# Kernel optimization log

Hardware: AMD Instinct MI355X
Metric: run time of the kernel (lower is better)

Reference implementation:

```python
import jax, jax.numpy as jnp
import numpy as np

N_NODES = 50000


def setup_inputs() -> dict:
    key = jax.random.key(0)
    k1, k2, k3, k4 = jax.random.split(key, 4)
    in_f, out_f = 128, 128
    n_edges = 625000
    x = jax.random.normal(k1, (N_NODES, in_f), dtype=jnp.float32)
    index = jax.random.randint(k2, (2, n_edges), 0, N_NODES, dtype=jnp.int64)
    # reset_parameters uses uniform(-1/sqrt(in), 1/sqrt(in))
    bound = 1.0 / np.sqrt(in_f)
    weight = jax.random.uniform(k3, (in_f, out_f), minval=-bound, maxval=bound, dtype=jnp.float32)
    bias = jax.random.uniform(k4, (out_f,), minval=-bound, maxval=bound, dtype=jnp.float32)
    return {"x": x, "index": index, "weight": weight, "bias": bias}


def reference(x, index, weight, bias):
    # F_out = D_hat^{-1/2} (A + I) D_hat^{-1/2} X W + b
    n = x.shape[0]
    loops = jnp.arange(n, dtype=index.dtype)
    src = jnp.concatenate([index[0], loops])  # [E + N]
    dst = jnp.concatenate([index[1], loops])
    # degrees of A_hat (counted on destination nodes)
    deg = jax.ops.segment_sum(jnp.ones_like(dst, dtype=x.dtype), dst, num_segments=n)
    dinv = jax.lax.rsqrt(jnp.maximum(deg, 1e-12))
    norm = dinv[src] * dinv[dst]  # [E + N]
    h = x @ weight  # [N, out] dense GEMM first (out <= in)
    msg = h[src] * norm[:, None]  # gather + scale
    out = jax.ops.segment_sum(msg, dst, num_segments=n)  # scatter-add
    return out + bias
```

## Files before the change

### kernel.cpp

```cpp
#include <hip/hip_runtime.h>

#define F    128
#define PAD  64
#define BKB  1024

typedef short short8 __attribute__((ext_vector_type(8)));
typedef float f32x4v __attribute__((ext_vector_type(4)));

__device__ __forceinline__ ushort f2bf(float f) {
    uint b = __float_as_uint(f);
    uint r = (b + 0x7fffu + ((b >> 16) & 1u)) >> 16;
    return (ushort)r;
}
__device__ __forceinline__ float bflo(uint v) { return __uint_as_float(v << 16); }
__device__ __forceinline__ float bfhi(uint v) { return __uint_as_float(v & 0xffff0000u); }


__global__ __launch_bounds__(256) void bucket(
    const int* __restrict__ src, const int* __restrict__ dst, int ne,
    int* __restrict__ cnt, ushort* __restrict__ padded, int n)
{
    const int xcd   = blockIdx.x & 7;
    const int slice = blockIdx.x >> 3;
    const int nsl   = BKB >> 3;
    int chunk = ((ne + nsl - 1) / nsl + 3) & ~3;
    const int sh  = (n + 7) >> 3;
    const int dlo = xcd * sh;
    const int dhi = (dlo + sh) < n ? (dlo + sh) : n;
    const int base = slice * chunk;
    const int lim  = (base + chunk) < ne ? (base + chunk) : ne;

    for (int e0 = base + threadIdx.x * 4; e0 < lim; e0 += 1024) {
        if (e0 + 3 < lim) {
            int4 s4 = *reinterpret_cast<const int4*>(&src[e0]);
            int4 d4 = *reinterpret_cast<const int4*>(&dst[e0]);
            if (d4.x >= dlo && d4.x < dhi) {
                int p = atomicAdd(&cnt[d4.x], 1);
                if (p < PAD) padded[(size_t)d4.x * PAD + p] = (ushort)s4.x;
            }
            if (d4.y >= dlo && d4.y < dhi) {
                int p = atomicAdd(&cnt[d4.y], 1);
                if (p < PAD) padded[(size_t)d4.y * PAD + p] = (ushort)s4.y;
            }
            if (d4.z >= dlo && d4.z < dhi) {
                int p = atomicAdd(&cnt[d4.z], 1);
                if (p < PAD) padded[(size_t)d4.z * PAD + p] = (ushort)s4.z;
            }
            if (d4.w >= dlo && d4.w < dhi) {
                int p = atomicAdd(&cnt[d4.w], 1);
                if (p < PAD) padded[(size_t)d4.w * PAD + p] = (ushort)s4.w;
            }
        } else {
            for (int e = e0; e < lim; ++e) {
                int d = dst[e];
                if (d >= dlo && d < dhi) {
                    int p = atomicAdd(&cnt[d], 1);
                    if (p < PAD) padded[(size_t)d * PAD + p] = (ushort)src[e];
                }
            }
        }
    }
}


__global__ __launch_bounds__(256) void gemm(
    const float* __restrict__ x, const float* __restrict__ w,
    ushort* __restrict__ g, int n)
{
    const int t    = threadIdx.x;
    const int lane = t & 63;
    const int wv   = t >> 6;
    const int wr   = wv >> 1, wc = wv & 1;
    const int l15  = lane & 15, kg = lane >> 4;
    const int row0 = blockIdx.x * 64 + wr * 32;
    const int col0 = wc * 64;

    f32x4v acc[2][4];
    #pragma unroll
    for (int rt = 0; rt < 2; ++rt)
        #pragma unroll
        for (int ct = 0; ct < 4; ++ct)
            acc[rt][ct] = (f32x4v){0.f, 0.f, 0.f, 0.f};

    #pragma unroll
    for (int kt = 0; kt < 4; ++kt) {
        const int k0 = kt * 32 + kg * 8;
        short8 a[2];
        #pragma unroll
        for (int rt = 0; rt < 2; ++rt) {
            int row = row0 + rt * 16 + l15;
            row = row < n ? row : n - 1;
            float4 p0 = *reinterpret_cast<const float4*>(&x[(size_t)row * F + k0]);
            float4 p1 = *reinterpret_cast<const float4*>(&x[(size_t)row * F + k0 + 4]);
            ushort u[8] = {f2bf(p0.x), f2bf(p0.y), f2bf(p0.z), f2bf(p0.w),
                           f2bf(p1.x), f2bf(p1.y), f2bf(p1.z), f2bf(p1.w)};
            a[rt] = *reinterpret_cast<short8*>(u);
        }
        short8 b[4];
        #pragma unroll
        for (int ct = 0; ct < 4; ++ct) {
            int col = col0 + ct * 16 + l15;
            ushort u[8];
            #pragma unroll
            for (int j = 0; j < 8; ++j)
                u[j] = f2bf(w[(size_t)(k0 + j) * F + col]);
            b[ct] = *reinterpret_cast<short8*>(u);
        }
        #pragma unroll
        for (int rt = 0; rt < 2; ++rt)
            #pragma unroll
            for (int ct = 0; ct < 4; ++ct)
                acc[rt][ct] = __builtin_amdgcn_mfma_f32_16x16x32_bf16(
                    a[rt], b[ct], acc[rt][ct], 0, 0, 0);
    }

    #pragma unroll
    for (int rt = 0; rt < 2; ++rt) {
        int rbase = row0 + rt * 16 + kg * 4;
        #pragma unroll
        for (int ct = 0; ct < 4; ++ct) {
            int col = col0 + ct * 16 + l15;
            #pragma unroll
            for (int rr = 0; rr < 4; ++rr) {
                int row = rbase + rr;
                if (row < n)
                    g[(size_t)row * F + col] = f2bf(acc[rt][ct][rr]);
            }
        }
    }
}


__global__ __launch_bounds__(256) void gather_bf16(
    const int* __restrict__ cnt, const ushort* __restrict__ padded,
    const ushort* __restrict__ g, const float* __restrict__ bias,
    float* __restrict__ out, int n)
{
    int wid  = (blockIdx.x * 256 + threadIdx.x) >> 6;
    int lane = threadIdx.x & 63;
    if (wid >= n) return;
    wid = __builtin_amdgcn_readfirstlane(wid);
    const int c = lane * 2;

    int   cv = cnt[wid];
    float dv = rsqrtf((float)cv + 1.0f);
    uint self = *reinterpret_cast<const uint*>(&g[(size_t)wid * F + c]);
    float ax = dv * bflo(self), ay = dv * bfhi(self);

    int m = cv < PAD ? cv : PAD;
    const ushort* pl = padded + (size_t)wid * PAD;

    int j = 0;
    for (; j + 4 <= m; j += 4) {
        int s0 = pl[j + 0], s1 = pl[j + 1], s2 = pl[j + 2], s3 = pl[j + 3];
        float d0 = rsqrtf((float)cnt[s0] + 1.0f);
        float d1 = rsqrtf((float)cnt[s1] + 1.0f);
        float d2 = rsqrtf((float)cnt[s2] + 1.0f);
        float d3 = rsqrtf((float)cnt[s3] + 1.0f);
        uint v0 = *reinterpret_cast<const uint*>(&g[(size_t)s0 * F + c]);
        uint v1 = *reinterpret_cast<const uint*>(&g[(size_t)s1 * F + c]);
        uint v2 = *reinterpret_cast<const uint*>(&g[(size_t)s2 * F + c]);
        uint v3 = *reinterpret_cast<const uint*>(&g[(size_t)s3 * F + c]);
        ax = fmaf(d0, bflo(v0), ax); ay = fmaf(d0, bfhi(v0), ay);
        ax = fmaf(d1, bflo(v1), ax); ay = fmaf(d1, bfhi(v1), ay);
        ax = fmaf(d2, bflo(v2), ax); ay = fmaf(d2, bfhi(v2), ay);
        ax = fmaf(d3, bflo(v3), ax); ay = fmaf(d3, bfhi(v3), ay);
    }
    for (; j < m; ++j) {
        int s = pl[j];
        float ds = rsqrtf((float)cnt[s] + 1.0f);
        uint v = *reinterpret_cast<const uint*>(&g[(size_t)s * F + c]);
        ax = fmaf(ds, bflo(v), ax);
        ay = fmaf(ds, bfhi(v), ay);
    }

    float2 bb = *reinterpret_cast<const float2*>(&bias[c]);
    float2 o;
    o.x = fmaf(dv, ax, bb.x);
    o.y = fmaf(dv, ay, bb.y);
    *reinterpret_cast<float2*>(&out[(size_t)wid * F + c]) = o;
}


__global__ __launch_bounds__(256) void gemm_scale(
    const float* __restrict__ x, const float* __restrict__ w,
    const float* __restrict__ dinv, float* __restrict__ g, int n)
{
    __shared__ float sWl[F * F];
    __shared__ float sXl[8][F];
    for (int i = threadIdx.x; i < F * F; i += 256) sWl[i] = w[i];
    __syncthreads();
    const int r  = threadIdx.x >> 5;
    const int cg = threadIdx.x & 31;
    for (int row0 = blockIdx.x * 8; row0 < n; row0 += gridDim.x * 8) {
        {
            int t4 = threadIdx.x * 4;
            int rr = t4 >> 7, cc = t4 & (F - 1);
            if (row0 + rr < n) {
                float4 v = *reinterpret_cast<const float4*>(&x[(size_t)(row0 + rr) * F + cc]);
                *reinterpret_cast<float4*>(&sXl[rr][cc]) = v;
            }
        }
        __syncthreads();
        int row = row0 + r;
        if (row < n) {
            float4 acc = make_float4(0.f, 0.f, 0.f, 0.f);
            const float* xr = sXl[r];
            #pragma unroll 8
            for (int k = 0; k < F; ++k) {
                float  xv = xr[k];
                float4 wv = *reinterpret_cast<const float4*>(&sWl[k * F + cg * 4]);
                acc.x = fmaf(xv, wv.x, acc.x);
                acc.y = fmaf(xv, wv.y, acc.y);
                acc.z = fmaf(xv, wv.z, acc.z);
                acc.w = fmaf(xv, wv.w, acc.w);
            }
            float s = dinv[row];
            acc.x *= s; acc.y *= s; acc.z *= s; acc.w *= s;
            *reinterpret_cast<float4*>(&g[(size_t)row * F + cg * 4]) = acc;
        }
        __syncthreads();
    }
}

__global__ void init_degf(float* __restrict__ deg, int n) {
    int i = blockIdx.x * blockDim.x + threadIdx.x;
    if (i < n) deg[i] = 1.0f;
}
__global__ void count_degf(const int* __restrict__ dst, int ne, float* __restrict__ deg) {
    int e = blockIdx.x * blockDim.x + threadIdx.x;
    if (e < ne) atomicAdd(&deg[dst[e]], 1.0f);
}
__global__ void calc_dinvf(const float* __restrict__ deg, float* __restrict__ dinv, int n) {
    int i = blockIdx.x * blockDim.x + threadIdx.x;
    if (i < n) dinv[i] = rsqrtf(fmaxf(deg[i], 1e-12f));
}
__global__ __launch_bounds__(256) void scatter_edges(
    const int* __restrict__ src, const int* __restrict__ dst, int ne,
    const float* __restrict__ g, float* __restrict__ out)
{
    int gid  = (blockIdx.x * blockDim.x + threadIdx.x) >> 5;
    int lane = threadIdx.x & 31;
    if (gid >= ne) return;
    int s = src[gid], d = dst[gid];
    float4 v = *reinterpret_cast<const float4*>(&g[(size_t)s * F + lane * 4]);
    float* op = &out[(size_t)d * F + lane * 4];
    atomicAdd(op + 0, v.x);
    atomicAdd(op + 1, v.y);
    atomicAdd(op + 2, v.z);
    atomicAdd(op + 3, v.w);
}
__global__ __launch_bounds__(256) void finalize(
    float* __restrict__ out, const float* __restrict__ g,
    const float* __restrict__ dinv, const float* __restrict__ bias, int n)
{
    int i = blockIdx.x * blockDim.x + threadIdx.x;
    if (i >= n * 32) return;
    int row = i >> 5, c4 = i & 31;
    float  s = dinv[row];
    float4 o = *reinterpret_cast<float4*>(&out[(size_t)i * 4]);
    float4 gg = *reinterpret_cast<const float4*>(&g[(size_t)i * 4]);
    float4 b = *reinterpret_cast<const float4*>(&bias[c4 * 4]);
    o.x = fmaf(s, o.x + gg.x, b.x);
    o.y = fmaf(s, o.y + gg.y, b.y);
    o.z = fmaf(s, o.z + gg.z, b.z);
    o.w = fmaf(s, o.w + gg.w, b.w);
    *reinterpret_cast<float4*>(&out[(size_t)i * 4]) = o;
}


extern "C" void kernel_launch(void* const* d_in, const int* in_sizes, int n_in,
                              void* d_out, int out_size, void* d_ws, size_t ws_size,
                              hipStream_t stream) {
    const float* x     = (const float*)d_in[0];
    const int*   index = (const int*)d_in[1];
    const float* w     = (const float*)d_in[2];
    const float* bias  = (const float*)d_in[3];
    float*       out   = (float*)d_out;

    int n  = in_sizes[0] / F;
    int ne = in_sizes[1] / 2;
    const int* src = index;
    const int* dst = index + ne;

    size_t b_cnt    = 0;
    size_t b_padded = (b_cnt + (size_t)n * 4 + 15) & ~(size_t)15;
    size_t b_g      = (b_padded + (size_t)n * PAD * 2 + 15) & ~(size_t)15;
    size_t need     = b_g + (size_t)n * F * 2;

    char* wsb = (char*)d_ws;
    int*    cnt    = (int*)(wsb + b_cnt);
    ushort* padded = (ushort*)(wsb + b_padded);
    ushort* g      = (ushort*)(wsb + b_g);

    int nbG = (n + 63) / 64;

    if (ws_size >= need && n <= 65535) {
        hipMemsetAsync(cnt, 0, (size_t)n * 4, stream);
        bucket<<<BKB, 256, 0, stream>>>(src, dst, ne, cnt, padded, n);
        gemm<<<nbG, 256, 0, stream>>>(x, w, g, n);
        int gb = (int)(((long long)n * 64 + 255) / 256);
        gather_bf16<<<gb, 256, 0, stream>>>(cnt, padded, g, bias, out, n);
    } else {
        float* degf  = (float*)wsb;
        float* dinvf = (float*)wsb + n;
        float* gf    = (float*)wsb + 2 * n;
        int nb  = (n + 255) / 256;
        int nbE = (ne + 255) / 256;
        hipMemsetAsync(d_out, 0, (size_t)out_size * sizeof(float), stream);
        init_degf<<<nb, 256, 0, stream>>>(degf, n);
        count_degf<<<nbE, 256, 0, stream>>>(dst, ne, degf);
        calc_dinvf<<<nb, 256, 0, stream>>>(degf, dinvf, n);
        gemm_scale<<<(n + 7) / 8, 256, 0, stream>>>(x, w, dinvf, gf, n);
        int sc_blocks = (int)(((long long)ne * 32 + 255) / 256);
        scatter_edges<<<sc_blocks, 256, 0, stream>>>(src, dst, ne, gf, out);
        finalize<<<(n * 32 + 255) / 256, 256, 0, stream>>>(out, gf, dinvf, bias, n);
    }
}
```

Baseline: 95.13 us.

## Fuse bucket and GEMM kernels into one launch; use nontemporal loads and stores

Merges the edge-bucketing kernel and the bf16 MFMA GEMM into a single hybrid kernel. The first nbB blocks do bucketing over fixed 8192-edge chunks and the rest do the GEMM, so the two independent phases can overlap and one launch is saved. It also switches the streaming edge and x loads, and the g and out stores, to nontemporal variants to reduce cache pollution. Chunk sizing changes the number of bucket blocks, and the memory-bound bucket blocks may contend with the GEMM blocks.

```diff
diff --git a/kernel.cpp b/kernel.cpp
--- a/kernel.cpp
+++ b/kernel.cpp
@@ -1,11 +1,13 @@
 #include <hip/hip_runtime.h>
 
-#define F    128
-#define PAD  64
-#define BKB  1024
+#define F     128
+#define PAD   64
+#define CHUNK 8192
 
 typedef short short8 __attribute__((ext_vector_type(8)));
 typedef float f32x4v __attribute__((ext_vector_type(4)));
+typedef float f32x2v __attribute__((ext_vector_type(2)));
+typedef int   i32x4v __attribute__((ext_vector_type(4)));
 
 __device__ __forceinline__ ushort f2bf(float f) {
     uint b = __float_as_uint(f);
@@ -16,63 +18,62 @@
 __device__ __forceinline__ float bfhi(uint v) { return __uint_as_float(v & 0xffff0000u); }
 
 
-__global__ __launch_bounds__(256) void bucket(
+__global__ __launch_bounds__(256) void hybrid(
     const int* __restrict__ src, const int* __restrict__ dst, int ne,
-    int* __restrict__ cnt, ushort* __restrict__ padded, int n)
-{
-    const int xcd   = blockIdx.x & 7;
-    const int slice = blockIdx.x >> 3;
-    const int nsl   = BKB >> 3;
-    int chunk = ((ne + nsl - 1) / nsl + 3) & ~3;
-    const int sh  = (n + 7) >> 3;
-    const int dlo = xcd * sh;
-    const int dhi = (dlo + sh) < n ? (dlo + sh) : n;
-    const int base = slice * chunk;
-    const int lim  = (base + chunk) < ne ? (base + chunk) : ne;
-
-    for (int e0 = base + threadIdx.x * 4; e0 < lim; e0 += 1024) {
-        if (e0 + 3 < lim) {
-            int4 s4 = *reinterpret_cast<const int4*>(&src[e0]);
-            int4 d4 = *reinterpret_cast<const int4*>(&dst[e0]);
-            if (d4.x >= dlo && d4.x < dhi) {
-                int p = atomicAdd(&cnt[d4.x], 1);
-                if (p < PAD) padded[(size_t)d4.x * PAD + p] = (ushort)s4.x;
-            }
-            if (d4.y >= dlo && d4.y < dhi) {
-                int p = atomicAdd(&cnt[d4.y], 1);
-                if (p < PAD) padded[(size_t)d4.y * PAD + p] = (ushort)s4.y;
-            }
-            if (d4.z >= dlo && d4.z < dhi) {
-                int p = atomicAdd(&cnt[d4.z], 1);
-                if (p < PAD) padded[(size_t)d4.z * PAD + p] = (ushort)s4.z;
-            }
-            if (d4.w >= dlo && d4.w < dhi) {
-                int p = atomicAdd(&cnt[d4.w], 1);
-                if (p < PAD) padded[(size_t)d4.w * PAD + p] = (ushort)s4.w;
-            }
-        } else {
-            for (int e = e0; e < lim; ++e) {
-                int d = dst[e];
-                if (d >= dlo && d < dhi) {
-                    int p = atomicAdd(&cnt[d], 1);
-                    if (p < PAD) padded[(size_t)d * PAD + p] = (ushort)src[e];
-                }
-            }
-        }
-    }
-}
-
-
-__global__ __launch_bounds__(256) void gemm(
+    int* __restrict__ cnt, ushort* __restrict__ padded, int nbB,
     const float* __restrict__ x, const float* __restrict__ w,
     ushort* __restrict__ g, int n)
 {
+    if (blockIdx.x < nbB) {
+        const int grp = blockIdx.x >> 3;
+        const int xcd = blockIdx.x & 7;
+        const int sh  = (n + 7) >> 3;
+        const int dlo = xcd * sh;
+        const int dhi = (dlo + sh) < n ? (dlo + sh) : n;
+        const int base = grp * CHUNK;
+        const int lim  = (base + CHUNK) < ne ? (base + CHUNK) : ne;
+        for (int e0 = base + threadIdx.x * 4; e0 < lim; e0 += 1024) {
+            if (e0 + 3 < lim) {
+                i32x4v s4 = __builtin_nontemporal_load(
+                    reinterpret_cast<const i32x4v*>(&src[e0]));
+                i32x4v d4 = __builtin_nontemporal_load(
+                    reinterpret_cast<const i32x4v*>(&dst[e0]));
+                if (d4.x >= dlo && d4.x < dhi) {
+                    int p = atomicAdd(&cnt[d4.x], 1);
+                    if (p < PAD) padded[(size_t)d4.x * PAD + p] = (ushort)s4.x;
+                }
+                if (d4.y >= dlo && d4.y < dhi) {
+                    int p = atomicAdd(&cnt[d4.y], 1);
+                    if (p < PAD) padded[(size_t)d4.y * PAD + p] = (ushort)s4.y;
+                }
+                if (d4.z >= dlo && d4.z < dhi) {
+                    int p = atomicAdd(&cnt[d4.z], 1);
+                    if (p < PAD) padded[(size_t)d4.z * PAD + p] = (ushort)s4.z;
+                }
+                if (d4.w >= dlo && d4.w < dhi) {
+                    int p = atomicAdd(&cnt[d4.w], 1);
+                    if (p < PAD) padded[(size_t)d4.w * PAD + p] = (ushort)s4.w;
+                }
+            } else {
+                for (int e = e0; e < lim; ++e) {
+                    int d = dst[e];
+                    if (d >= dlo && d < dhi) {
+                        int p = atomicAdd(&cnt[d], 1);
+                        if (p < PAD) padded[(size_t)d * PAD + p] = (ushort)src[e];
+                    }
+                }
+            }
+        }
+        return;
+    }
+
+    const int gb   = blockIdx.x - nbB;
     const int t    = threadIdx.x;
     const int lane = t & 63;
     const int wv   = t >> 6;
     const int wr   = wv >> 1, wc = wv & 1;
     const int l15  = lane & 15, kg = lane >> 4;
-    const int row0 = blockIdx.x * 64 + wr * 32;
+    const int row0 = gb * 64 + wr * 32;
     const int col0 = wc * 64;
 
     f32x4v acc[2][4];
@@ -90,8 +91,10 @@
         for (int rt = 0; rt < 2; ++rt) {
             int row = row0 + rt * 16 + l15;
             row = row < n ? row : n - 1;
-            float4 p0 = *reinterpret_cast<const float4*>(&x[(size_t)row * F + k0]);
-            float4 p1 = *reinterpret_cast<const float4*>(&x[(size_t)row * F + k0 + 4]);
+            f32x4v p0 = __builtin_nontemporal_load(
+                reinterpret_cast<const f32x4v*>(&x[(size_t)row * F + k0]));
+            f32x4v p1 = __builtin_nontemporal_load(
+                reinterpret_cast<const f32x4v*>(&x[(size_t)row * F + k0 + 4]));
             ushort u[8] = {f2bf(p0.x), f2bf(p0.y), f2bf(p0.z), f2bf(p0.w),
                            f2bf(p1.x), f2bf(p1.y), f2bf(p1.z), f2bf(p1.w)};
             a[rt] = *reinterpret_cast<short8*>(u);
@@ -124,7 +127,8 @@
             for (int rr = 0; rr < 4; ++rr) {
                 int row = rbase + rr;
                 if (row < n)
-                    g[(size_t)row * F + col] = f2bf(acc[rt][ct][rr]);
+                    __builtin_nontemporal_store(f2bf(acc[rt][ct][rr]),
+                                                &g[(size_t)row * F + col]);
             }
         }
     }
@@ -175,10 +179,10 @@
     }
 
     float2 bb = *reinterpret_cast<const float2*>(&bias[c]);
-    float2 o;
+    f32x2v o;
     o.x = fmaf(dv, ax, bb.x);
     o.y = fmaf(dv, ay, bb.y);
-    *reinterpret_cast<float2*>(&out[(size_t)wid * F + c]) = o;
+    __builtin_nontemporal_store(o, reinterpret_cast<f32x2v*>(&out[(size_t)wid * F + c]));
 }
 
 
@@ -293,12 +297,12 @@
     ushort* padded = (ushort*)(wsb + b_padded);
     ushort* g      = (ushort*)(wsb + b_g);
 
+    int nbB = ((ne + CHUNK - 1) / CHUNK) * 8;
     int nbG = (n + 63) / 64;
 
     if (ws_size >= need && n <= 65535) {
         hipMemsetAsync(cnt, 0, (size_t)n * 4, stream);
-        bucket<<<BKB, 256, 0, stream>>>(src, dst, ne, cnt, padded, n);
-        gemm<<<nbG, 256, 0, stream>>>(x, w, g, n);
+        hybrid<<<nbB + nbG, 256, 0, stream>>>(src, dst, ne, cnt, padded, nbB, x, w, g, n);
         int gb = (int)(((long long)n * 64 + 255) / 256);
         gather_bf16<<<gb, 256, 0, stream>>>(cnt, padded, g, bias, out, n);
     } else {
```

New measurement: 99.49 us. 1.05x slower.
